# Kernel optimization log

Hardware: AMD Instinct MI355X
Metric: run time of the kernel (lower is better)

The kernel has to match this reference:

```python
import jax, jax.numpy as jnp
import numpy as np

S, B, H = 2048, 32, 1024

def setup_inputs() -> dict:
    key = jax.random.key(0)
    k1, k2, k3, k4, k5 = jax.random.split(key, 5)
    stdv = 1.0 / np.sqrt(2 * H)  # nn.Linear default init scale (approx, uniform in torch)
    return {
        "hidden": jax.random.normal(k1, (1, B, H), dtype=jnp.float32),
        "encoder_outputs": jax.random.normal(k2, (S, B, H), dtype=jnp.float32),
        "W": jax.random.normal(k3, (H, 2 * H), dtype=jnp.float32) * stdv,
        "b": jax.random.normal(k4, (H,), dtype=jnp.float32) * stdv,
        "v": jax.random.normal(k5, (H,), dtype=jnp.float32) * (1.0 / np.sqrt(H)),
    }

def reference(hidden, encoder_outputs, W, b, v):
    # hidden: (1, B, H); encoder_outputs: (S, B, H)
    h = hidden[0]                              # (B, H)
    e = jnp.swapaxes(encoder_outputs, 0, 1)    # (B, S, H)
    Wh, We = W[:, :H], W[:, H:]                # split concat-linear: cat([H_rep, enc]) @ W^T
    # energy = tanh(Linear(cat([H, enc], -1)))  -> (B, S, H)
    pre_h = h @ Wh.T                           # (B, H), broadcast over S (H is repeated per step)
    pre_e = jnp.einsum('bsh,kh->bsk', e, We)   # (B, S, H)
    energy = jnp.tanh(pre_e + pre_h[:, None, :] + b)
    scores = jnp.einsum('bsk,k->bs', energy, v)  # v-dot per position -> (B, S)
    return jax.nn.softmax(scores, axis=1)[:, None, :]  # (B, 1, S)
```

## Files before the change

kernel.cpp:

```cpp
#include <hip/hip_runtime.h>


typedef __attribute__((ext_vector_type(8))) short short8;
typedef __attribute__((ext_vector_type(4))) float floatx4;
typedef __attribute__((ext_vector_type(4))) unsigned int uint4v;

#define GLDS(g, l) __builtin_amdgcn_global_load_lds( \
    (const __attribute__((address_space(1))) void*)(g), \
    (__attribute__((address_space(3))) void*)(l), 16, 0, 0)

__device__ __forceinline__ unsigned pack2(float lo, float hi) {
  union { float f; unsigned u; } a, b; a.f = lo; b.f = hi;
  return __builtin_amdgcn_perm(b.u + 0x8000u, a.u + 0x8000u, 0x07060302u);
}

__device__ __forceinline__ unsigned cvt_pk(float lo, float hi) {
  unsigned r;
  asm("v_cvt_pk_bf16_f32 %0, %1, %2" : "=v"(r) : "v"(lo), "v"(hi));
  return r;
}

__device__ __forceinline__ float fast_tanh(float x) {
  float e = __expf(2.0f * x);
  return 1.0f - 2.0f / (e + 1.0f);
}

__global__ __launch_bounds__(256) void k_cvtB(
    const float* __restrict__ W, unsigned int* __restrict__ Bw2,
    float* __restrict__ scoresT) {
  const int idx = blockIdx.x * 256 + threadIdx.x;
  const int kc = idx >> 10, n = idx & 1023;
  const float* src = W + (size_t)n * 2048 + 1024 + kc * 8;
  float4 f0 = *(const float4*)(src);
  float4 f1 = *(const float4*)(src + 4);
  uint4v u = {pack2(f0.x, f0.y), pack2(f0.z, f0.w),
              pack2(f1.x, f1.y), pack2(f1.z, f1.w)};
  *(uint4v*)(Bw2 + ((size_t)kc * 8192 + n * 8) / 2) = u;
  if (idx < 65536) scoresT[idx] = 0.f;
}

__global__ __launch_bounds__(256) void k_preh(
    const float* __restrict__ hidden, const float* __restrict__ W,
    const float* __restrict__ bias, float* __restrict__ tpre) {
  const int g  = blockIdx.x * 256 + threadIdx.x;
  const int b  = g & 31;
  const int ko = g >> 5;
  const float* wr = W + (size_t)ko * 2048;
  const float* hr = hidden + b * 1024;
  float s = 0.f;
  #pragma unroll 8
  for (int j = 0; j < 1024; j += 4) {
    float4 wv = *(const float4*)(wr + j);
    float4 hv = *(const float4*)(hr + j);
    s += wv.x * hv.x + wv.y * hv.y + wv.z * hv.z + wv.w * hv.w;
  }
  tpre[b * 1024 + ko] = s + bias[ko];
}

__device__ __forceinline__ void mma_tile(const short* __restrict__ Asb,
                                         const short* __restrict__ Bsb,
                                         int wm, int wn, int c, int q,
                                         floatx4 acc[4][4]) {
  #pragma unroll
  for (int ks = 0; ks < 2; ++ks) {
    short8 af[4], bf[4];
    #pragma unroll
    for (int mt = 0; mt < 4; ++mt) {
      const int row = wm * 64 + mt * 16 + c;
      af[mt] = *(const short8*)&Asb[row * 64 + (((ks * 4 + q) ^ (c & 7)) << 3)];
    }
    #pragma unroll
    for (int nt = 0; nt < 4; ++nt)
      bf[nt] = *(const short8*)&Bsb[(ks * 4 + q) * 1024 + (wn * 64 + nt * 16 + c) * 8];
    #pragma unroll
    for (int mt = 0; mt < 4; ++mt)
      #pragma unroll
      for (int nt = 0; nt < 4; ++nt)
        acc[mt][nt] = __builtin_amdgcn_mfma_f32_16x16x32_bf16(
            af[mt], bf[nt], acc[mt][nt], 0, 0, 0);
  }
}

__global__ __launch_bounds__(256, 2) void k_gemm(
    const float* __restrict__ A,
    const unsigned short* __restrict__ Bw2,
    const float* __restrict__ tpre,
    const float* __restrict__ vvec,
    float* __restrict__ scoresT) {
  __shared__ short As[2][128 * 64];
  __shared__ short Bs[2][8 * 128 * 8];

  const int l = blockIdx.x;
  const int x = l & 7, j = l >> 3;
  const int Mbase = (x * 64 + (j >> 3)) * 128;
  const int Nbase = (j & 7) * 128;

  const int tid = threadIdx.x, lane = tid & 63, w = tid >> 6;
  const int wm = w >> 1, wn = w & 1;
  const int c = lane & 15, q = lane >> 4;

  const int arow  = tid >> 2;
  const int ach   = (tid & 3) * 2;
  const int acolF = (tid & 3) * 16;
  const float* ap0 = A + (size_t)(Mbase + arow) * 1024 + acolF;
  const float* ap1 = ap0 + 64 * 1024;
  const int sw0 = (ach    ) ^ (arow & 7);
  const int sw1 = (ach + 1) ^ (arow & 7);

  const unsigned short* bgb = Bw2 + (size_t)(Nbase + lane) * 8;

  floatx4 acc[4][4];
  #pragma unroll
  for (int mt = 0; mt < 4; ++mt)
    #pragma unroll
    for (int nt = 0; nt < 4; ++nt) {
      floatx4 z = {0.f, 0.f, 0.f, 0.f};
      acc[mt][nt] = z;
    }

  {
    float4 g[2][4];
    #pragma unroll
    for (int h = 0; h < 2; ++h) {
      const float* ap = h ? ap1 : ap0;
      #pragma unroll
      for (int jj = 0; jj < 4; ++jj) g[h][jj] = *(const float4*)(ap + jj * 4);
    }
    #pragma unroll
    for (int i = 0; i < 4; ++i) {
      const int seg = w * 4 + i, kcl = seg >> 1, half = seg & 1;
      GLDS(bgb + ((size_t)kcl * 8192 + half * 512), &Bs[0][kcl * 1024 + half * 512]);
    }
    #pragma unroll
    for (int h = 0; h < 2; ++h) {
      short* base = &As[0][(arow + h * 64) * 64];
      uint4v u0 = {cvt_pk(g[h][0].x, g[h][0].y), cvt_pk(g[h][0].z, g[h][0].w),
                   cvt_pk(g[h][1].x, g[h][1].y), cvt_pk(g[h][1].z, g[h][1].w)};
      uint4v u1 = {cvt_pk(g[h][2].x, g[h][2].y), cvt_pk(g[h][2].z, g[h][2].w),
                   cvt_pk(g[h][3].x, g[h][3].y), cvt_pk(g[h][3].z, g[h][3].w)};
      *(uint4v*)&base[sw0 << 3] = u0;
      *(uint4v*)&base[sw1 << 3] = u1;
    }
  }
  __syncthreads();

  int cur = 0;
  for (int t = 0; t < 15; ++t) {
    const int nxt = cur ^ 1;
    const int k1 = (t + 1) * 64;

    float4 g[2][4];
    #pragma unroll
    for (int h = 0; h < 2; ++h) {
      const float* ap = h ? ap1 : ap0;
      #pragma unroll
      for (int jj = 0; jj < 4; ++jj) g[h][jj] = *(const float4*)(ap + k1 + jj * 4);
    }
    #pragma unroll
    for (int i = 0; i < 4; ++i) {
      const int seg = w * 4 + i, kcl = seg >> 1, half = seg & 1;
      GLDS(bgb + ((size_t)((k1 >> 3) + kcl) * 8192 + half * 512),
           &Bs[nxt][kcl * 1024 + half * 512]);
    }

    mma_tile(&As[cur][0], &Bs[cur][0], wm, wn, c, q, acc);

    #pragma unroll
    for (int h = 0; h < 2; ++h) {
      short* base = &As[nxt][(arow + h * 64) * 64];
      uint4v u0 = {cvt_pk(g[h][0].x, g[h][0].y), cvt_pk(g[h][0].z, g[h][0].w),
                   cvt_pk(g[h][1].x, g[h][1].y), cvt_pk(g[h][1].z, g[h][1].w)};
      uint4v u1 = {cvt_pk(g[h][2].x, g[h][2].y), cvt_pk(g[h][2].z, g[h][2].w),
                   cvt_pk(g[h][3].x, g[h][3].y), cvt_pk(g[h][3].z, g[h][3].w)};
      *(uint4v*)&base[sw0 << 3] = u0;
      *(uint4v*)&base[sw1 << 3] = u1;
    }
    __syncthreads();
    cur = nxt;
  }
  mma_tile(&As[cur][0], &Bs[cur][0], wm, wn, c, q, acc);

  const int mwave = Mbase + wm * 64;
  const int nwave = Nbase + wn * 64;
  float vv[4];
  #pragma unroll
  for (int nt = 0; nt < 4; ++nt) vv[nt] = vvec[nwave + nt * 16 + c];
  #pragma unroll
  for (int mt = 0; mt < 4; ++mt) {
    #pragma unroll
    for (int i = 0; i < 4; ++i) {
      const int mrow = mwave + mt * 16 + q * 4 + i;
      const float* tb = tpre + (mrow & 31) * 1024;
      float ssum = 0.f;
      #pragma unroll
      for (int nt = 0; nt < 4; ++nt) {
        float pre = acc[mt][nt][i] + tb[nwave + nt * 16 + c];
        ssum += fast_tanh(pre) * vv[nt];
      }
      #pragma unroll
      for (int off = 1; off < 16; off <<= 1) ssum += __shfl_xor(ssum, off, 64);
      if (c == 0) atomicAdd(&scoresT[(mrow & 31) * 2048 + (mrow >> 5)], ssum);
    }
  }
}

__global__ __launch_bounds__(256) void k_softmax(
    const float* __restrict__ scoresT, float* __restrict__ out) {
  const int b = blockIdx.x;
  const int t = threadIdx.x;
  const int w = t >> 6, lane = t & 63;
  __shared__ float red[4];
  float vals[8];
  float m = -3.0e38f;
  #pragma unroll
  for (int i = 0; i < 8; ++i) {
    vals[i] = scoresT[b * 2048 + t + 256 * i];
    m = fmaxf(m, vals[i]);
  }
  #pragma unroll
  for (int off = 32; off; off >>= 1) m = fmaxf(m, __shfl_xor(m, off, 64));
  if (lane == 0) red[w] = m;
  __syncthreads();
  m = fmaxf(fmaxf(red[0], red[1]), fmaxf(red[2], red[3]));
  __syncthreads();
  float e[8];
  float sum = 0.f;
  #pragma unroll
  for (int i = 0; i < 8; ++i) { e[i] = __expf(vals[i] - m); sum += e[i]; }
  #pragma unroll
  for (int off = 32; off; off >>= 1) sum += __shfl_xor(sum, off, 64);
  if (lane == 0) red[w] = sum;
  __syncthreads();
  sum = red[0] + red[1] + red[2] + red[3];
  const float inv = 1.0f / sum;
  #pragma unroll
  for (int i = 0; i < 8; ++i) out[b * 2048 + t + 256 * i] = e[i] * inv;
}

extern "C" void kernel_launch(void* const* d_in, const int* in_sizes, int n_in,
                              void* d_out, int out_size, void* d_ws, size_t ws_size,
                              hipStream_t stream) {
  const float* hidden = (const float*)d_in[0];
  const float* enc    = (const float*)d_in[1];
  const float* W      = (const float*)d_in[2];
  const float* bias   = (const float*)d_in[3];
  const float* vvec   = (const float*)d_in[4];
  float* out = (float*)d_out;

  float* scoresT = (float*)d_ws;
  float* tpre    = scoresT + 65536;
  unsigned int* Bw2 = (unsigned int*)(tpre + 32768);

  hipLaunchKernelGGL(k_cvtB, dim3(512), dim3(256), 0, stream, W, Bw2, scoresT);
  hipLaunchKernelGGL(k_preh, dim3(128), dim3(256), 0, stream, hidden, W, bias, tpre);
  hipLaunchKernelGGL(k_gemm, dim3(4096), dim3(256), 0, stream,
                     enc, (const unsigned short*)Bw2, tpre, vvec, scoresT);
  hipLaunchKernelGGL(k_softmax, dim3(32), dim3(256), 0, stream, scoresT, out);
}
```

Baseline: 663.7 us.

## Triple-buffer B tiles with two-stage-ahead direct-to-LDS prefetch and manual waitcnts

Moves the B operand (weights) to a three-slot LDS ring and issues its global-to-LDS loads two K-steps ahead instead of one. The A operand stays double-buffered. __syncthreads is replaced with explicit vmcnt/lgkmcnt waits plus s_barrier, so the next-next B tile's loads can stay in flight across the barrier. The aim is to hide more global latency behind the MFMA work. The cost is 16KB more LDS, which may cut occupancy below 2 blocks per CU, and the hand-counted vmcnt values must be right or correctness breaks.

```diff
diff --git a/kernel.cpp b/kernel.cpp
--- a/kernel.cpp
+++ b/kernel.cpp
@@ -87,8 +87,8 @@
     const float* __restrict__ tpre,
     const float* __restrict__ vvec,
     float* __restrict__ scoresT) {
-  __shared__ short As[2][128 * 64];
-  __shared__ short Bs[2][8 * 128 * 8];
+  __shared__ short Asf[2 * 128 * 64];
+  __shared__ short Bsf[3 * 8 * 128 * 8];
 
   const int l = blockIdx.x;
   const int x = l & 7, j = l >> 3;
@@ -118,6 +118,9 @@
       acc[mt][nt] = z;
     }
 
+  int aOffC = 0, aOffN = 128 * 64;
+  int bOff0 = 0, bOff1 = 8192, bOff2 = 16384;
+
   {
     float4 g[2][4];
     #pragma unroll
@@ -129,11 +132,19 @@
     #pragma unroll
     for (int i = 0; i < 4; ++i) {
       const int seg = w * 4 + i, kcl = seg >> 1, half = seg & 1;
-      GLDS(bgb + ((size_t)kcl * 8192 + half * 512), &Bs[0][kcl * 1024 + half * 512]);
-    }
-    #pragma unroll
-    for (int h = 0; h < 2; ++h) {
-      short* base = &As[0][(arow + h * 64) * 64];
+      GLDS(bgb + ((size_t)kcl * 8192 + half * 512),
+           &Bsf[bOff0 + kcl * 1024 + half * 512]);
+    }
+    #pragma unroll
+    for (int i = 0; i < 4; ++i) {
+      const int seg = w * 4 + i, kcl = seg >> 1, half = seg & 1;
+      GLDS(bgb + ((size_t)(8 + kcl) * 8192 + half * 512),
+           &Bsf[bOff1 + kcl * 1024 + half * 512]);
+    }
+    asm volatile("s_waitcnt vmcnt(4)" ::: "memory");
+    #pragma unroll
+    for (int h = 0; h < 2; ++h) {
+      short* base = &Asf[aOffC + (arow + h * 64) * 64];
       uint4v u0 = {cvt_pk(g[h][0].x, g[h][0].y), cvt_pk(g[h][0].z, g[h][0].w),
                    cvt_pk(g[h][1].x, g[h][1].y), cvt_pk(g[h][1].z, g[h][1].w)};
       uint4v u1 = {cvt_pk(g[h][2].x, g[h][2].y), cvt_pk(g[h][2].z, g[h][2].w),
@@ -141,12 +152,12 @@
       *(uint4v*)&base[sw0 << 3] = u0;
       *(uint4v*)&base[sw1 << 3] = u1;
     }
-  }
-  __syncthreads();
-
-  int cur = 0;
+    asm volatile("s_waitcnt lgkmcnt(0)" ::: "memory");
+    __builtin_amdgcn_s_barrier();
+    asm volatile("" ::: "memory");
+  }
+
   for (int t = 0; t < 15; ++t) {
-    const int nxt = cur ^ 1;
     const int k1 = (t + 1) * 64;
 
     float4 g[2][4];
@@ -156,18 +167,24 @@
       #pragma unroll
       for (int jj = 0; jj < 4; ++jj) g[h][jj] = *(const float4*)(ap + k1 + jj * 4);
     }
-    #pragma unroll
-    for (int i = 0; i < 4; ++i) {
-      const int seg = w * 4 + i, kcl = seg >> 1, half = seg & 1;
-      GLDS(bgb + ((size_t)((k1 >> 3) + kcl) * 8192 + half * 512),
-           &Bs[nxt][kcl * 1024 + half * 512]);
-    }
-
-    mma_tile(&As[cur][0], &Bs[cur][0], wm, wn, c, q, acc);
-
-    #pragma unroll
-    for (int h = 0; h < 2; ++h) {
-      short* base = &As[nxt][(arow + h * 64) * 64];
+    if (t <= 13) {
+      const int k2 = (t + 2) * 64;
+      #pragma unroll
+      for (int i = 0; i < 4; ++i) {
+        const int seg = w * 4 + i, kcl = seg >> 1, half = seg & 1;
+        GLDS(bgb + ((size_t)((k2 >> 3) + kcl) * 8192 + half * 512),
+             &Bsf[bOff2 + kcl * 1024 + half * 512]);
+      }
+    }
+
+    mma_tile(&Asf[aOffC], &Bsf[bOff0], wm, wn, c, q, acc);
+
+    if (t <= 13) asm volatile("s_waitcnt vmcnt(4)" ::: "memory");
+    else         asm volatile("s_waitcnt vmcnt(0)" ::: "memory");
+
+    #pragma unroll
+    for (int h = 0; h < 2; ++h) {
+      short* base = &Asf[aOffN + (arow + h * 64) * 64];
       uint4v u0 = {cvt_pk(g[h][0].x, g[h][0].y), cvt_pk(g[h][0].z, g[h][0].w),
                    cvt_pk(g[h][1].x, g[h][1].y), cvt_pk(g[h][1].z, g[h][1].w)};
       uint4v u1 = {cvt_pk(g[h][2].x, g[h][2].y), cvt_pk(g[h][2].z, g[h][2].w),
@@ -175,10 +192,14 @@
       *(uint4v*)&base[sw0 << 3] = u0;
       *(uint4v*)&base[sw1 << 3] = u1;
     }
-    __syncthreads();
-    cur = nxt;
-  }
-  mma_tile(&As[cur][0], &Bs[cur][0], wm, wn, c, q, acc);
+    asm volatile("s_waitcnt lgkmcnt(0)" ::: "memory");
+    __builtin_amdgcn_s_barrier();
+    asm volatile("" ::: "memory");
+
+    int ta = aOffC; aOffC = aOffN; aOffN = ta;
+    int tb = bOff0; bOff0 = bOff1; bOff1 = bOff2; bOff2 = tb;
+  }
+  mma_tile(&Asf[aOffC], &Bsf[bOff0], wm, wn, c, q, acc);
 
   const int mwave = Mbase + wm * 64;
   const int nwave = Nbase + wn * 64;
```

New measurement: 677.4 us. +2.1%, slower.
